# Optimization experiments

Hardware: AMD Instinct MI355X
Metric: run time of the kernel (lower is better)

Reference implementation:

```python
import jax, jax.numpy as jnp
import numpy as np


def setup_inputs() -> dict:
    key = jax.random.key(0)
    k1, k2, k3 = jax.random.split(key, 3)
    B, D, N, C = 4096, 256, 65536, 10
    x = jax.random.normal(k1, (B, D), dtype=jnp.float32)
    keys = jax.random.normal(k2, (N, D), dtype=jnp.float32)
    values = jax.random.uniform(k3, (N, C), dtype=jnp.float32)
    return {"x": x, "keys": keys, "values": values, "k": 8}


def reference(x, keys, values, k):
    # squared euclidean distances [B, N] without materializing diff cube:
    x_sq = jnp.sum(x * x, axis=1, keepdims=True)          # [B,1]
    k_sq = jnp.sum(keys * keys, axis=1)                   # [N]
    dists = x_sq - 2.0 * (x @ keys.T) + k_sq[None, :]     # [B,N]
    neg_top, indices = jax.lax.top_k(-dists, k)           # [B,k]
    hit_values = values[indices]                          # [B,k,C]
    return jnp.sum(hit_values, axis=1) / jnp.float32(k)   # [B,C]
```

## Files before the change

kernel.cpp:

```cpp
#include <hip/hip_runtime.h>
#include <stdint.h>
#include <float.h>

#define B_ROWS 4096
#define N_KEYS 65536
#define DDIM 256
#define NCH 10

#define NSPLIT 16
#define SPLIT_KEYS (N_KEYS / NSPLIT)
#define ROWS_PER_BLK 128
#define CHUNK_KEYS 32
#define NCHUNK (SPLIT_KEYS / CHUNK_KEYS)

typedef float f32x4 __attribute__((ext_vector_type(4)));
typedef short bf16x8 __attribute__((ext_vector_type(8)));

static __device__ __forceinline__ unsigned short f2bf(float f) {
  unsigned u = __float_as_uint(f);
  return (unsigned short)((u + 0x7FFFu + ((u >> 16) & 1u)) >> 16);
}
static __device__ __forceinline__ unsigned ford(float f) {
  unsigned u = __float_as_uint(f);
  return u ^ ((unsigned)((int)u >> 31) | 0x80000000u);
}
static __device__ __forceinline__ unsigned long long shfl_xor_u64(unsigned long long v, int m) {
  unsigned lo = __shfl_xor((unsigned)v, m, 64);
  unsigned hi = __shfl_xor((unsigned)(v >> 32), m, 64);
  return ((unsigned long long)hi << 32) | lo;
}
static __device__ __forceinline__ double shfl_xor_f64(double v, int m) {
  return __longlong_as_double((long long)shfl_xor_u64((unsigned long long)__double_as_longlong(v), m));
}
static __device__ __forceinline__ void gl_lds16(const void* g, void* l) {
  __builtin_amdgcn_global_load_lds(
      (const __attribute__((address_space(1))) unsigned int*)g,
      (__attribute__((address_space(3))) unsigned int*)l, 16, 0, 0);
}

__global__ __launch_bounds__(256) void transpose_keys(const float* __restrict__ keys,
                                                      unsigned char* __restrict__ kbf,
                                                      float* __restrict__ ksq) {
  __shared__ __align__(16) unsigned char T[128 * 512];
  const int t = threadIdx.x;
  const int lane = t & 63;
  const float4* src = (const float4*)(keys + (size_t)blockIdx.x * 128 * DDIM);
#pragma unroll
  for (int j = 0; j < 32; ++j) {
    int g = j * 256 + t;
    float4 v = src[g];
    int key = g >> 6;
    int u = lane >> 1, sub = lane & 1;
    unsigned lo = ((unsigned)f2bf(v.y) << 16) | f2bf(v.x);
    unsigned hi2 = ((unsigned)f2bf(v.w) << 16) | f2bf(v.z);
    unsigned long long p = ((unsigned long long)hi2 << 32) | lo;
    *(unsigned long long*)&T[key * 512 + ((u ^ (key & 7)) << 4) + (sub << 3)] = p;
    float ss = v.x * v.x + v.y * v.y + v.z * v.z + v.w * v.w;
#pragma unroll
    for (int off = 32; off; off >>= 1) ss += __shfl_xor(ss, off, 64);
    if (lane == 0) ksq[blockIdx.x * 128 + key] = ss;
  }
  __syncthreads();
  uint4* dst = (uint4*)kbf + (size_t)blockIdx.x * 4096;
#pragma unroll
  for (int j = 0; j < 16; ++j) {
    int ou = j * 256 + t;
    int rec = ou >> 10, rem = ou & 1023;
    int koct = rem >> 5, key32 = rem & 31;
    int keyl = rec * 32 + key32;
    dst[ou] = *(const uint4*)&T[keyl * 512 + ((koct ^ (keyl & 7)) << 4)];
  }
}

__global__ __launch_bounds__(512, 4) void knn_main(
    const float* __restrict__ x,
    const unsigned char* __restrict__ kbf,
    const float* __restrict__ ksqg,
    unsigned int* __restrict__ pools,
    unsigned int* __restrict__ counts,
    int CAP) {
  __shared__ __align__(16) unsigned char tiles[4][16384];
  __shared__ float tauh[2][4][16][2];
  __shared__ unsigned int rowcnt[128];

  const int t = threadIdx.x;
  const int lane = t & 63;
  const int wv = t >> 6;
  const int mw = wv & 1;
  const int ws = wv >> 1;
  const int lo4 = lane & 15;
  const int hi = lane >> 4;

  const int split = blockIdx.x & (NSPLIT - 1);
  const int rb = (blockIdx.x >> 4) * ROWS_PER_BLK;
  const int sb = split * SPLIT_KEYS;

  const int xrow0 = rb + ws * 32 + lo4;
  const int xrow1 = xrow0 + 16;
  const int rl0 = ws * 32 + lo4, rl1 = rl0 + 16;

  bf16x8 xb0[8], xb1[8];
#pragma unroll
  for (int s = 0; s < 8; ++s) {
    const float* p0 = x + (size_t)xrow0 * DDIM + s * 32 + hi * 8;
    const float* p1 = x + (size_t)xrow1 * DDIM + s * 32 + hi * 8;
    float4 a = *(const float4*)p0, b = *(const float4*)(p0 + 4);
    float4 c = *(const float4*)p1, d = *(const float4*)(p1 + 4);
    union { unsigned short us[8]; bf16x8 v; } u0, u1;
    u0.us[0]=f2bf(-2.f*a.x); u0.us[1]=f2bf(-2.f*a.y); u0.us[2]=f2bf(-2.f*a.z); u0.us[3]=f2bf(-2.f*a.w);
    u0.us[4]=f2bf(-2.f*b.x); u0.us[5]=f2bf(-2.f*b.y); u0.us[6]=f2bf(-2.f*b.z); u0.us[7]=f2bf(-2.f*b.w);
    u1.us[0]=f2bf(-2.f*c.x); u1.us[1]=f2bf(-2.f*c.y); u1.us[2]=f2bf(-2.f*c.z); u1.us[3]=f2bf(-2.f*c.w);
    u1.us[4]=f2bf(-2.f*d.x); u1.us[5]=f2bf(-2.f*d.y); u1.us[6]=f2bf(-2.f*d.z); u1.us[7]=f2bf(-2.f*d.w);
    xb0[s] = u0.v; xb1[s] = u1.v;
  }

  if (t < 128) rowcnt[t] = 0;

  float smin0 = FLT_MAX, smin1 = FLT_MAX;
  const unsigned char* srcbase = kbf + ((size_t)(split * NCHUNK) << 14);
  const size_t pb0 = ((size_t)xrow0 * NSPLIT + split) * (size_t)CAP;
  const size_t pb1 = ((size_t)xrow1 * NSPLIT + split) * (size_t)CAP;

  auto STAGE = [&](int c, int buf) {
    const unsigned char* src = srcbase + ((size_t)c << 14);
#pragma unroll
    for (int i = 0; i < 2; ++i)
      gl_lds16(src + (((i * 512) + t) << 4),
               (unsigned char*)tiles[buf] + ((i * 512 + wv * 64) << 4));
  };
  auto LOADQ = [&](int c) {
    return *(const float4*)(ksqg + sb + c * CHUNK_KEYS + mw * 16 + hi * 4);
  };

  f32x4 a0, a1;
  float4 kqc, kqn;

  auto COMPUTE = [&](int buf) {
    const unsigned char* tile = tiles[buf];
    f32x4 ini;
    ini[0] = kqc.x; ini[1] = kqc.y; ini[2] = kqc.z; ini[3] = kqc.w;
    a0 = ini; a1 = ini;
    __builtin_amdgcn_s_setprio(1);
#pragma unroll
    for (int s = 0; s < 8; ++s) {
      const unsigned char* rp = tile + (s * 4 + hi) * 512 + (mw * 16 + lo4) * 16;
      bf16x8 af = *(const bf16x8*)rp;
      a0 = __builtin_amdgcn_mfma_f32_16x16x32_bf16(af, xb0[s], a0, 0, 0, 0);
      a1 = __builtin_amdgcn_mfma_f32_16x16x32_bf16(af, xb1[s], a1, 0, 0, 0);
    }
    __builtin_amdgcn_s_setprio(0);
  };

  auto SEL = [&](int c, bool append, float tau0, float tau1) {
    float mb0 = fminf(fminf(a0[0], a0[1]), fminf(a0[2], a0[3]));
    float mb1 = fminf(fminf(a1[0], a1[1]), fminf(a1[2], a1[3]));
    smin0 = fminf(smin0, mb0);
    smin1 = fminf(smin1, mb1);
    if (append) {
      const int kloc = c * CHUNK_KEYS + mw * 16 + hi * 4;
      if (mb0 <= tau0) {
#pragma unroll
        for (int i = 0; i < 4; ++i) {
          if (a0[i] <= tau0) {
            unsigned slot = atomicAdd(&rowcnt[rl0], 1u);
            if ((int)slot < CAP)
              pools[pb0 + slot] = (ford(a0[i]) & 0xFFFFF000u) | (unsigned)(kloc + i);
          }
        }
      }
      if (mb1 <= tau1) {
#pragma unroll
        for (int i = 0; i < 4; ++i) {
          if (a1[i] <= tau1) {
            unsigned slot = atomicAdd(&rowcnt[rl1], 1u);
            if ((int)slot < CAP)
              pools[pb1 + slot] = (ford(a1[i]) & 0xFFFFF000u) | (unsigned)(kloc + i);
          }
        }
      }
    }
  };

  auto RDTAU = [&](float& tau0, float& tau1) {
    tau0 = fmaxf(tauh[0][ws][lo4][0], tauh[0][ws][lo4][1]);
    tau1 = fmaxf(tauh[1][ws][lo4][0], tauh[1][ws][lo4][1]);
  };

  auto PUBLISH = [&]() {
    float p0 = fmaxf(smin0, __shfl_xor(smin0, 16, 64));
    p0 = fmaxf(p0, __shfl_xor(p0, 32, 64));
    float p1 = fmaxf(smin1, __shfl_xor(smin1, 16, 64));
    p1 = fmaxf(p1, __shfl_xor(p1, 32, 64));
    if (hi == 0) {
      tauh[0][ws][lo4][mw] = p0;
      tauh[1][ws][lo4][mw] = p1;
    }
  };

  STAGE(0, 0);
  STAGE(64, 1);
  __syncthreads();
  kqc = LOADQ(0);
  COMPUTE(0); SEL(0, false, 0.f, 0.f);
  kqc = LOADQ(64);
  COMPUTE(1); SEL(64, false, 0.f, 0.f);
  PUBLISH();
  __syncthreads();
  STAGE(1, 1);
  STAGE(2, 2);
  kqc = LOADQ(0);
  kqn = LOADQ(1);

#pragma unroll 1
  for (int c = 0; c < NCHUNK; ++c) {
    asm volatile("s_waitcnt vmcnt(4)" ::: "memory");
    __builtin_amdgcn_s_barrier();
    float tau0, tau1;
    RDTAU(tau0, tau1);
    COMPUTE(c & 3);
    SEL(c, true, tau0, tau1);
    if (c & 1) PUBLISH();
    kqc = kqn;
    kqn = LOADQ((c + 2 < NCHUNK) ? c + 2 : 0);
    const int cs = (c + 3 < NCHUNK) ? c + 3 : c + 3 - NCHUNK;
    STAGE(cs, (c + 3) & 3);
  }

  __syncthreads();
  if (t < 128) counts[(size_t)(rb + t) * NSPLIT + split] = rowcnt[t];
}

__global__ __launch_bounds__(64) void knn_refine(
    const float* __restrict__ x,
    const float* __restrict__ keys,
    const float* __restrict__ ksq,
    const float* __restrict__ values,
    const unsigned int* __restrict__ pools,
    const unsigned int* __restrict__ counts,
    int CAP,
    float* __restrict__ out) {
  __shared__ float4 xl[64];
  const int row = blockIdx.x;
  const int lane = threadIdx.x;

  xl[lane] = ((const float4*)(x + (size_t)row * DDIM))[lane];
  __syncthreads();

  unsigned long long h[8];
#pragma unroll
  for (int i = 0; i < 8; ++i) h[i] = ~0ULL;

  auto insert = [&](unsigned long long v) {
    if (v < h[7]) {
#pragma unroll
      for (int j = 7; j >= 1; --j) {
        unsigned long long a = h[j - 1];
        unsigned long long mx = a > v ? a : v;
        h[j] = (v < h[j]) ? mx : h[j];
      }
      h[0] = h[0] < v ? h[0] : v;
    }
  };

  for (int s = 0; s < NSPLIT; ++s) {
    unsigned cnt = counts[(size_t)row * NSPLIT + s];
    if ((int)cnt <= CAP) {
      const unsigned int* pp = pools + ((size_t)row * NSPLIT + s) * (size_t)CAP;
      for (int i = lane; i < (int)cnt; i += 64) {
        unsigned p = pp[i];
        unsigned gk = (unsigned)(s * SPLIT_KEYS) + (p & 0xFFFu);
        insert(((unsigned long long)(p & 0xFFFFF000u) << 16) | gk);
      }
    } else {
      for (int kk = lane; kk < SPLIT_KEYS; kk += 64) {
        int gk = s * SPLIT_KEYS + kk;
        const float4* kr = (const float4*)(keys + (size_t)gk * DDIM);
        float acc = 0.f;
#pragma unroll 8
        for (int d = 0; d < 64; ++d) {
          float4 kv = kr[d], xv = xl[d];
          acc = fmaf(kv.x, xv.x, acc); acc = fmaf(kv.y, xv.y, acc);
          acc = fmaf(kv.z, xv.z, acc); acc = fmaf(kv.w, xv.w, acc);
        }
        float sc = fmaf(-2.0f, acc, ksq[gk]);
        insert(((unsigned long long)(ford(sc) & 0xFFFFF000u) << 16) | (unsigned)gk);
      }
    }
  }

  int myidx = 0;
#pragma unroll 1
  for (int r = 0; r < 24; ++r) {
    unsigned long long m = h[0];
#pragma unroll
    for (int off = 32; off; off >>= 1) {
      unsigned long long o = shfl_xor_u64(m, off);
      m = o < m ? o : m;
    }
    if (lane == r) myidx = (int)(m & 0xFFFFu);
    if (h[0] == m) {
#pragma unroll
      for (int i = 0; i < 7; ++i) h[i] = h[i + 1];
      h[7] = ~0ULL;
    }
  }

  double dv = 1e300;
  if (lane < 24) {
    const float4* kr = (const float4*)(keys + (size_t)myidx * DDIM);
    double s = 0.0;
#pragma unroll 8
    for (int d = 0; d < 64; ++d) {
      float4 kv = kr[d], xv = xl[d];
      double d0 = (double)xv.x - (double)kv.x;
      double d1 = (double)xv.y - (double)kv.y;
      double d2 = (double)xv.z - (double)kv.z;
      double d3 = (double)xv.w - (double)kv.w;
      s += d0 * d0 + d1 * d1 + d2 * d2 + d3 * d3;
    }
    dv = s;
  }

  int di = myidx;
  int chosen[8];
#pragma unroll
  for (int r = 0; r < 8; ++r) {
    double m = dv; int mi = di;
#pragma unroll
    for (int off = 32; off; off >>= 1) {
      double om = shfl_xor_f64(m, off);
      int omi = __shfl_xor(mi, off, 64);
      if (om < m || (om == m && omi < mi)) { m = om; mi = omi; }
    }
    chosen[r] = mi;
    if (di == mi && dv < 1e300) dv = 1e300;
  }

  if (lane < NCH) {
    double a = 0.0;
#pragma unroll
    for (int r = 0; r < 8; ++r) a += (double)values[(size_t)chosen[r] * NCH + lane];
    out[row * NCH + lane] = (float)(a * 0.125);
  }
}

extern "C" void kernel_launch(void* const* d_in, const int* in_sizes, int n_in,
                              void* d_out, int out_size, void* d_ws, size_t ws_size,
                              hipStream_t stream) {
  (void)in_sizes; (void)n_in; (void)out_size;
  const float* x      = (const float*)d_in[0];
  const float* keys   = (const float*)d_in[1];
  const float* values = (const float*)d_in[2];
  float* out = (float*)d_out;

  char* ws = (char*)d_ws;
  unsigned char* kbf = (unsigned char*)ws;
  float* ksq   = (float*)(ws + 33554432);
  unsigned int* counts = (unsigned int*)(ws + 33554432 + 262144);
  unsigned int* pools  = (unsigned int*)(ws + 33554432 + 262144 + 262144);

  size_t base = 33554432 + 262144 + 262144;
  size_t cap = (ws_size > base) ? (ws_size - base) / ((size_t)B_ROWS * NSPLIT * 4) : 60;
  if (cap < 60) cap = 60;
  if (cap > 512) cap = 512;
  int CAP = (int)cap;

  transpose_keys<<<N_KEYS / 128, 256, 0, stream>>>(keys, kbf, ksq);
  knn_main<<<(B_ROWS / ROWS_PER_BLK) * NSPLIT, 512, 0, stream>>>(
      x, kbf, ksq, pools, counts, CAP);
  knn_refine<<<B_ROWS, 64, 0, stream>>>(x, keys, ksq, values, pools, counts, CAP, out);
}
```

Measured before the change: 276.3 us.

## Switch to 32x32x16 MFMA with 64-key chunks and double-buffered staging

```diff
diff --git a/kernel.cpp b/kernel.cpp
--- a/kernel.cpp
+++ b/kernel.cpp
@@ -10,10 +10,11 @@
 #define NSPLIT 16
 #define SPLIT_KEYS (N_KEYS / NSPLIT)
 #define ROWS_PER_BLK 128
-#define CHUNK_KEYS 32
+#define CHUNK_KEYS 64
 #define NCHUNK (SPLIT_KEYS / CHUNK_KEYS)
 
 typedef float f32x4 __attribute__((ext_vector_type(4)));
+typedef float f32x16 __attribute__((ext_vector_type(16)));
 typedef short bf16x8 __attribute__((ext_vector_type(8)));
 
 static __device__ __forceinline__ unsigned short f2bf(float f) {
@@ -79,8 +80,8 @@
     unsigned int* __restrict__ pools,
     unsigned int* __restrict__ counts,
     int CAP) {
-  __shared__ __align__(16) unsigned char tiles[4][16384];
-  __shared__ float tauh[2][4][16][2];
+  __shared__ __align__(16) unsigned char tiles[2][32768];
+  __shared__ float tauh[2][4][32];
   __shared__ unsigned int rowcnt[128];
 
   const int t = threadIdx.x;
@@ -88,142 +89,112 @@
   const int wv = t >> 6;
   const int mw = wv & 1;
   const int ws = wv >> 1;
-  const int lo4 = lane & 15;
-  const int hi = lane >> 4;
+  const int col = lane & 31;
+  const int hi5 = lane >> 5;
 
   const int split = blockIdx.x & (NSPLIT - 1);
   const int rb = (blockIdx.x >> 4) * ROWS_PER_BLK;
   const int sb = split * SPLIT_KEYS;
 
-  const int xrow0 = rb + ws * 32 + lo4;
-  const int xrow1 = xrow0 + 16;
-  const int rl0 = ws * 32 + lo4, rl1 = rl0 + 16;
-
-  bf16x8 xb0[8], xb1[8];
-#pragma unroll
-  for (int s = 0; s < 8; ++s) {
-    const float* p0 = x + (size_t)xrow0 * DDIM + s * 32 + hi * 8;
-    const float* p1 = x + (size_t)xrow1 * DDIM + s * 32 + hi * 8;
-    float4 a = *(const float4*)p0, b = *(const float4*)(p0 + 4);
-    float4 c = *(const float4*)p1, d = *(const float4*)(p1 + 4);
-    union { unsigned short us[8]; bf16x8 v; } u0, u1;
-    u0.us[0]=f2bf(-2.f*a.x); u0.us[1]=f2bf(-2.f*a.y); u0.us[2]=f2bf(-2.f*a.z); u0.us[3]=f2bf(-2.f*a.w);
-    u0.us[4]=f2bf(-2.f*b.x); u0.us[5]=f2bf(-2.f*b.y); u0.us[6]=f2bf(-2.f*b.z); u0.us[7]=f2bf(-2.f*b.w);
-    u1.us[0]=f2bf(-2.f*c.x); u1.us[1]=f2bf(-2.f*c.y); u1.us[2]=f2bf(-2.f*c.z); u1.us[3]=f2bf(-2.f*c.w);
-    u1.us[4]=f2bf(-2.f*d.x); u1.us[5]=f2bf(-2.f*d.y); u1.us[6]=f2bf(-2.f*d.z); u1.us[7]=f2bf(-2.f*d.w);
-    xb0[s] = u0.v; xb1[s] = u1.v;
+  const int xrow = rb + ws * 32 + col;
+  const int rl = ws * 32 + col;
+
+  bf16x8 xb[16];
+#pragma unroll
+  for (int s = 0; s < 16; ++s) {
+    const float* p = x + (size_t)xrow * DDIM + s * 16 + hi5 * 8;
+    float4 a = *(const float4*)p, b = *(const float4*)(p + 4);
+    union { unsigned short us[8]; bf16x8 v; } u;
+    u.us[0]=f2bf(-2.f*a.x); u.us[1]=f2bf(-2.f*a.y); u.us[2]=f2bf(-2.f*a.z); u.us[3]=f2bf(-2.f*a.w);
+    u.us[4]=f2bf(-2.f*b.x); u.us[5]=f2bf(-2.f*b.y); u.us[6]=f2bf(-2.f*b.z); u.us[7]=f2bf(-2.f*b.w);
+    xb[s] = u.v;
   }
 
   if (t < 128) rowcnt[t] = 0;
 
-  float smin0 = FLT_MAX, smin1 = FLT_MAX;
-  const unsigned char* srcbase = kbf + ((size_t)(split * NCHUNK) << 14);
-  const size_t pb0 = ((size_t)xrow0 * NSPLIT + split) * (size_t)CAP;
-  const size_t pb1 = ((size_t)xrow1 * NSPLIT + split) * (size_t)CAP;
+  float sminA = FLT_MAX, sminB = FLT_MAX;
+  const unsigned char* srcbase = kbf + (size_t)sb * 512;
+  const size_t pb = ((size_t)xrow * NSPLIT + split) * (size_t)CAP;
 
   auto STAGE = [&](int c, int buf) {
-    const unsigned char* src = srcbase + ((size_t)c << 14);
-#pragma unroll
-    for (int i = 0; i < 2; ++i)
+    const unsigned char* src = srcbase + ((size_t)c << 15);
+#pragma unroll
+    for (int i = 0; i < 4; ++i)
       gl_lds16(src + (((i * 512) + t) << 4),
                (unsigned char*)tiles[buf] + ((i * 512 + wv * 64) << 4));
   };
-  auto LOADQ = [&](int c) {
-    return *(const float4*)(ksqg + sb + c * CHUNK_KEYS + mw * 16 + hi * 4);
-  };
-
-  f32x4 a0, a1;
-  float4 kqc, kqn;
-
-  auto COMPUTE = [&](int buf) {
-    const unsigned char* tile = tiles[buf];
-    f32x4 ini;
-    ini[0] = kqc.x; ini[1] = kqc.y; ini[2] = kqc.z; ini[3] = kqc.w;
-    a0 = ini; a1 = ini;
+
+  f32x16 acc;
+
+  auto COMPUTE = [&](int c, int buf) {
+    const float* kq = ksqg + sb + c * CHUNK_KEYS + mw * 32 + hi5 * 4;
+    float4 q0 = *(const float4*)(kq);
+    float4 q1 = *(const float4*)(kq + 8);
+    float4 q2 = *(const float4*)(kq + 16);
+    float4 q3 = *(const float4*)(kq + 24);
+    acc[0]=q0.x; acc[1]=q0.y; acc[2]=q0.z; acc[3]=q0.w;
+    acc[4]=q1.x; acc[5]=q1.y; acc[6]=q1.z; acc[7]=q1.w;
+    acc[8]=q2.x; acc[9]=q2.y; acc[10]=q2.z; acc[11]=q2.w;
+    acc[12]=q3.x; acc[13]=q3.y; acc[14]=q3.z; acc[15]=q3.w;
+    const unsigned char* rec = tiles[buf] + mw * 16384 + col * 16;
     __builtin_amdgcn_s_setprio(1);
 #pragma unroll
-    for (int s = 0; s < 8; ++s) {
-      const unsigned char* rp = tile + (s * 4 + hi) * 512 + (mw * 16 + lo4) * 16;
-      bf16x8 af = *(const bf16x8*)rp;
-      a0 = __builtin_amdgcn_mfma_f32_16x16x32_bf16(af, xb0[s], a0, 0, 0, 0);
-      a1 = __builtin_amdgcn_mfma_f32_16x16x32_bf16(af, xb1[s], a1, 0, 0, 0);
+    for (int s = 0; s < 16; ++s) {
+      bf16x8 af = *(const bf16x8*)(rec + (2 * s + hi5) * 512);
+      acc = __builtin_amdgcn_mfma_f32_32x32x16_bf16(af, xb[s], acc, 0, 0, 0);
     }
     __builtin_amdgcn_s_setprio(0);
   };
 
-  auto SEL = [&](int c, bool append, float tau0, float tau1) {
-    float mb0 = fminf(fminf(a0[0], a0[1]), fminf(a0[2], a0[3]));
-    float mb1 = fminf(fminf(a1[0], a1[1]), fminf(a1[2], a1[3]));
-    smin0 = fminf(smin0, mb0);
-    smin1 = fminf(smin1, mb1);
-    if (append) {
-      const int kloc = c * CHUNK_KEYS + mw * 16 + hi * 4;
-      if (mb0 <= tau0) {
-#pragma unroll
-        for (int i = 0; i < 4; ++i) {
-          if (a0[i] <= tau0) {
-            unsigned slot = atomicAdd(&rowcnt[rl0], 1u);
-            if ((int)slot < CAP)
-              pools[pb0 + slot] = (ford(a0[i]) & 0xFFFFF000u) | (unsigned)(kloc + i);
-          }
+  auto SEL = [&](int c, bool append, float tau) {
+    float m0 = fminf(fminf(fminf(acc[0], acc[1]), fminf(acc[2], acc[3])),
+                     fminf(fminf(acc[4], acc[5]), fminf(acc[6], acc[7])));
+    float m1 = fminf(fminf(fminf(acc[8], acc[9]), fminf(acc[10], acc[11])),
+                     fminf(fminf(acc[12], acc[13]), fminf(acc[14], acc[15])));
+    sminA = fminf(sminA, m0);
+    sminB = fminf(sminB, m1);
+    if (append && fminf(m0, m1) <= tau) {
+      const int kbase = c * CHUNK_KEYS + mw * 32 + 4 * hi5;
+#pragma unroll
+      for (int r = 0; r < 16; ++r) {
+        float sc = acc[r];
+        if (sc <= tau) {
+          int key = kbase + (r & 3) + 8 * (r >> 2);
+          unsigned slot = atomicAdd(&rowcnt[rl], 1u);
+          if ((int)slot < CAP)
+            pools[pb + slot] = (ford(sc) & 0xFFFFF000u) | (unsigned)key;
         }
       }
-      if (mb1 <= tau1) {
-#pragma unroll
-        for (int i = 0; i < 4; ++i) {
-          if (a1[i] <= tau1) {
-            unsigned slot = atomicAdd(&rowcnt[rl1], 1u);
-            if ((int)slot < CAP)
-              pools[pb1 + slot] = (ford(a1[i]) & 0xFFFFF000u) | (unsigned)(kloc + i);
-          }
-        }
-      }
-    }
-  };
-
-  auto RDTAU = [&](float& tau0, float& tau1) {
-    tau0 = fmaxf(tauh[0][ws][lo4][0], tauh[0][ws][lo4][1]);
-    tau1 = fmaxf(tauh[1][ws][lo4][0], tauh[1][ws][lo4][1]);
+    }
   };
 
   auto PUBLISH = [&]() {
-    float p0 = fmaxf(smin0, __shfl_xor(smin0, 16, 64));
-    p0 = fmaxf(p0, __shfl_xor(p0, 32, 64));
-    float p1 = fmaxf(smin1, __shfl_xor(smin1, 16, 64));
-    p1 = fmaxf(p1, __shfl_xor(p1, 32, 64));
-    if (hi == 0) {
-      tauh[0][ws][lo4][mw] = p0;
-      tauh[1][ws][lo4][mw] = p1;
-    }
+    float l = fmaxf(sminA, sminB);
+    l = fmaxf(l, __shfl_xor(l, 32, 64));
+    if (hi5 == 0) tauh[mw][ws][col] = l;
+  };
+  auto RDTAU = [&]() {
+    return fmaxf(tauh[0][ws][col], tauh[1][ws][col]);
   };
 
   STAGE(0, 0);
-  STAGE(64, 1);
-  __syncthreads();
-  kqc = LOADQ(0);
-  COMPUTE(0); SEL(0, false, 0.f, 0.f);
-  kqc = LOADQ(64);
-  COMPUTE(1); SEL(64, false, 0.f, 0.f);
+  STAGE(32, 1);
+  __syncthreads();
+  COMPUTE(0, 0);  SEL(0, false, 0.f);
+  COMPUTE(32, 1); SEL(32, false, 0.f);
   PUBLISH();
   __syncthreads();
-  STAGE(1, 1);
-  STAGE(2, 2);
-  kqc = LOADQ(0);
-  kqn = LOADQ(1);
 
 #pragma unroll 1
   for (int c = 0; c < NCHUNK; ++c) {
     asm volatile("s_waitcnt vmcnt(4)" ::: "memory");
     __builtin_amdgcn_s_barrier();
-    float tau0, tau1;
-    RDTAU(tau0, tau1);
-    COMPUTE(c & 3);
-    SEL(c, true, tau0, tau1);
+    const int cs = (c + 1 < NCHUNK) ? c + 1 : 0;
+    STAGE(cs, (c + 1) & 1);
+    float tau = RDTAU();
+    COMPUTE(c, c & 1);
+    SEL(c, true, tau);
     if (c & 1) PUBLISH();
-    kqc = kqn;
-    kqn = LOADQ((c + 2 < NCHUNK) ? c + 2 : 0);
-    const int cs = (c + 3 < NCHUNK) ? c + 3 : c + 3 - NCHUNK;
-    STAGE(cs, (c + 3) & 3);
   }
 
   __syncthreads();
```

Result: slower. 302.2 us (+9.4%).

## Process chunk pairs per iteration with one barrier and restructured prefetch

Applied to the files above, without the earlier changes.

```diff
diff --git a/kernel.cpp b/kernel.cpp
--- a/kernel.cpp
+++ b/kernel.cpp
@@ -133,12 +133,11 @@
   };
 
   f32x4 a0, a1;
-  float4 kqc, kqn;
-
-  auto COMPUTE = [&](int buf) {
+
+  auto COMPUTE = [&](int buf, float4 kq) {
     const unsigned char* tile = tiles[buf];
     f32x4 ini;
-    ini[0] = kqc.x; ini[1] = kqc.y; ini[2] = kqc.z; ini[3] = kqc.w;
+    ini[0] = kq.x; ini[1] = kq.y; ini[2] = kq.z; ini[3] = kq.w;
     a0 = ini; a1 = ini;
     __builtin_amdgcn_s_setprio(1);
 #pragma unroll
@@ -200,30 +199,41 @@
   STAGE(0, 0);
   STAGE(64, 1);
   __syncthreads();
-  kqc = LOADQ(0);
-  COMPUTE(0); SEL(0, false, 0.f, 0.f);
-  kqc = LOADQ(64);
-  COMPUTE(1); SEL(64, false, 0.f, 0.f);
+  {
+    float4 q = LOADQ(0);
+    COMPUTE(0, q); SEL(0, false, 0.f, 0.f);
+    q = LOADQ(64);
+    COMPUTE(1, q); SEL(64, false, 0.f, 0.f);
+  }
   PUBLISH();
   __syncthreads();
+
   STAGE(1, 1);
-  STAGE(2, 2);
-  kqc = LOADQ(0);
-  kqn = LOADQ(1);
+  __builtin_amdgcn_sched_barrier(0);
+  float4 kqc0 = LOADQ(0);
+  float4 kqc1 = LOADQ(1);
+  float4 kqn0, kqn1;
 
 #pragma unroll 1
-  for (int c = 0; c < NCHUNK; ++c) {
-    asm volatile("s_waitcnt vmcnt(4)" ::: "memory");
+  for (int p = 0; p < NCHUNK / 2; ++p) {
+    const int c0 = 2 * p, c1 = c0 + 1;
+    asm volatile("s_waitcnt vmcnt(2)" ::: "memory");
     __builtin_amdgcn_s_barrier();
+    const int n0 = (c0 + 2 < NCHUNK) ? c0 + 2 : 0;
+    const int n1 = (c1 + 2 < NCHUNK) ? c1 + 2 : 1;
+    STAGE(n0, (c0 + 2) & 3);
+    STAGE(n1, (c1 + 2) & 3);
+    __builtin_amdgcn_sched_barrier(0);
+    kqn0 = LOADQ(n0);
+    kqn1 = LOADQ(n1);
     float tau0, tau1;
     RDTAU(tau0, tau1);
-    COMPUTE(c & 3);
-    SEL(c, true, tau0, tau1);
-    if (c & 1) PUBLISH();
-    kqc = kqn;
-    kqn = LOADQ((c + 2 < NCHUNK) ? c + 2 : 0);
-    const int cs = (c + 3 < NCHUNK) ? c + 3 : c + 3 - NCHUNK;
-    STAGE(cs, (c + 3) & 3);
+    COMPUTE(c0 & 3, kqc0);
+    SEL(c0, true, tau0, tau1);
+    COMPUTE(c1 & 3, kqc1);
+    SEL(c1, true, tau0, tau1);
+    PUBLISH();
+    kqc0 = kqn0; kqc1 = kqn1;
   }
 
   __syncthreads();
```

Result: slower. 287.3 us (+4.0%).
